# Performance work log

Measured on AMD Instinct MI355X. Metric: run time of the kernel, lower is better.

## Reference

```python
import jax, jax.numpy as jnp
import numpy as np

PATCH = 3  # patch_size=3, stride=1
B, C, H, W = 8, 256, 64, 64


def _extract_patches(x):
    # x: (c, h, w) -> (c*PATCH*PATCH, N) with N = (h-2)*(w-2), valid 3x3 patches
    c, h, w = x.shape
    hh, ww = h - PATCH + 1, w - PATCH + 1
    pats = jnp.stack([x[:, i:i + hh, j:j + ww]
                      for i in range(PATCH) for j in range(PATCH)], axis=0)  # (9, c, hh, ww)
    return pats.reshape(PATCH * PATCH * c, hh * ww)


def _index_to_flow(max_idx):
    # max_idx: (hh, ww) int -> flow (h, w, 2) padded by 2 at bottom/right
    hh, ww = max_idx.shape
    flow_w = (max_idx % ww).astype(jnp.float32)
    flow_h = (max_idx // ww).astype(jnp.float32)
    gy, gx = jnp.meshgrid(jnp.arange(hh, dtype=jnp.float32),
                          jnp.arange(ww, dtype=jnp.float32), indexing='ij')
    flow = jnp.stack((flow_w - gx, flow_h - gy), axis=2)  # (hh, ww, 2)
    return jnp.pad(flow, ((0, 2), (0, 2), (0, 0)))


def _per_image(feat_in, feat_ref):
    c, h, w = feat_in.shape
    hh, ww = h - PATCH + 1, w - PATCH + 1
    # channel-wise L2 normalize each spatial position (F.normalize dim=0, eps=1e-12)
    feat_in = feat_in / jnp.maximum(jnp.linalg.norm(feat_in, axis=0, keepdims=True), 1e-12)
    feat_ref = feat_ref / jnp.maximum(jnp.linalg.norm(feat_ref, axis=0, keepdims=True), 1e-12)
    Pi = _extract_patches(feat_in)    # (k, N)
    Pr = _extract_patches(feat_ref)   # (k, N)
    # is_norm=True: normalize ref patches (norm + 1e-5, per BasicSR feature_match_index)
    Pr = Pr / (jnp.linalg.norm(Pr, axis=0, keepdims=True) + 1e-5)
    corr = Pi.T @ Pr                  # (N, N) exhaustive patch correlation
    max_val = corr.max(axis=1)
    max_idx = jnp.argmax(corr, axis=1)
    # norm_input=True: divide by input patch norms
    max_val = max_val / jnp.linalg.norm(Pi, axis=0)
    max_val = max_val.reshape(hh, ww)
    max_idx = max_idx.reshape(hh, ww)
    sim = jnp.pad(max_val, ((1, 1), (1, 1)))[None]  # (1, h, w)
    flow = _index_to_flow(max_idx)                   # (h, w, 2)
    # nine down-right shifts (fill 0 at top-left), tensor_shift semantics
    shifted = jnp.stack([jnp.pad(flow[:h - i, :w - j], ((i, 0), (j, 0), (0, 0)))
                         for i in range(3) for j in range(3)], axis=0)  # (9, h, w, 2)
    return flow, shifted, sim


def setup_inputs() -> dict:
    key = jax.random.key(0)
    k1, k2 = jax.random.split(key)
    features1 = jax.random.normal(k1, (B, C, H, W), dtype=jnp.float32)
    features2 = jax.random.normal(k2, (B, C, H, W), dtype=jnp.float32)
    return {"features1": features1, "features2": features2}


def reference(features1, features2):
    pre_flow, pre_offset, pre_similarity = jax.vmap(_per_image)(features1, features2)
    # pre_flow: (b,h,w,2); pre_offset: (b,9,h,w,2); pre_similarity: (b,1,h,w)
    return pre_flow, pre_offset, pre_similarity
```

## Files before the change

kernel.cpp:

```cpp
#include <hip/hip_runtime.h>

typedef unsigned short u16;
typedef unsigned char u8;
typedef unsigned int u32;
typedef __bf16 bf16x8 __attribute__((ext_vector_type(8)));
typedef float f32x4 __attribute__((ext_vector_type(4)));

constexpr int BATCH = 8;
constexpr int C = 256;
constexpr int H = 64;
constexpr int W = 64;
constexpr int HW = H * W;
constexpr int HH = 62, WW = 62;
constexpr int NQ = HH * WW;
constexpr int SEG = 8;
constexpr int NBLK_RED = 536;

constexpr size_t OFF_RNORM = 0;
constexpr size_t OFF_RESV = 262144;
constexpr size_t OFF_RESI = 385280;
constexpr size_t OFF_SLOT0 = 508416;
constexpr size_t SP_H1 = 0;
constexpr size_t SP_L1 = 2097152;
constexpr size_t SP_H2 = 4194304;
constexpr size_t SP_L2 = 6291456;
constexpr size_t SP_P = 8388608;
constexpr size_t SP_PIDX8 = 75497472;
constexpr size_t SLOT_BYTES = 77594624;

typedef const __attribute__((address_space(1))) unsigned int* gas_ptr;
typedef __attribute__((address_space(3))) unsigned int* las_ptr;
__device__ __forceinline__ void gl16(const void* g, void* l) {
  __builtin_amdgcn_global_load_lds((gas_ptr)g, (las_ptr)l, 16, 0, 0);
}

__device__ __forceinline__ int pre_of(int ki) {
  if (ki <= 62) return ki * (ki + 1) / 2;
  int r = 123 - ki;
  return 1953 + 1891 - r * (r + 1) / 2;
}

__global__ __launch_bounds__(256) void norm_kernel(const float* __restrict__ f1,
                                                   const float* __restrict__ f2,
                                                   float* __restrict__ rnorm) {
  int by = blockIdx.x;
  int tensor = blockIdx.y;
  const float* f = tensor ? f2 : f1;
  int b = by >> 6, y = by & 63;
  int x = threadIdx.x & 63;
  int cq = threadIdx.x >> 6;
  const float* base = f + ((size_t)b * C) * HW + y * W + x;
  float s = 0.f;
  for (int c = cq; c < C; c += 4) {
    float v = base[(size_t)c * HW];
    s = fmaf(v, v, s);
  }
  __shared__ float sm[4][64];
  sm[cq][x] = s;
  __syncthreads();
  if (threadIdx.x < 64) {
    float t = sm[0][x] + sm[1][x] + sm[2][x] + sm[3][x];
    float nrm = fmaxf(sqrtf(t), 1e-12f);
    rnorm[((size_t)tensor * BATCH + b) * HW + y * W + x] = 1.0f / nrm;
  }
}

__global__ __launch_bounds__(256) void convert_kernel(const float* __restrict__ f1,
                                                      const float* __restrict__ f2,
                                                      const float* __restrict__ rnorm,
                                                      int b0, char* __restrict__ slot0) {
  int chunk = blockIdx.x;
  int tensor = blockIdx.y;
  int sloti = blockIdx.z;
  int bi = b0 + sloti;
  char* slot = slot0 + (size_t)sloti * SLOT_BYTES;
  int pos0 = chunk * 32;
  const float* f = (tensor ? f2 : f1) + (size_t)bi * C * HW;
  const float* rn = rnorm + ((size_t)tensor * BATCH + bi) * HW + pos0;
  u16* dh = (u16*)(slot + (tensor ? SP_H2 : SP_H1)) + (size_t)pos0 * C;
  u16* dl = (u16*)(slot + (tensor ? SP_L2 : SP_L1)) + (size_t)pos0 * C;

  __shared__ u32 sm[32][257];
  int t = threadIdx.x;
  int px = t & 31, cg = t >> 5;
  float r = rn[px];
  for (int kk = 0; kk < 32; ++kk) {
    int c = (cg << 5) + kk;
    float v = f[(size_t)c * HW + pos0 + px] * r;
    __bf16 h = (__bf16)v;
    float hf = (float)h;
    __bf16 lo = (__bf16)(v - hf);
    sm[px][c] = ((u32)__builtin_bit_cast(u16, h) << 16) | (u32)__builtin_bit_cast(u16, lo);
  }
  __syncthreads();
  int px2 = t >> 3, seg = t & 7;
  int c0 = seg * 32;
  for (int g8 = 0; g8 < 4; ++g8) {
    u32 hw0, hw1, hw2, hw3, lw0, lw1, lw2, lw3;
    u32 a, b2;
    a = sm[px2][c0 + g8 * 8 + 0]; b2 = sm[px2][c0 + g8 * 8 + 1];
    hw0 = (a >> 16) | (b2 & 0xFFFF0000u); lw0 = (a & 0xFFFFu) | (b2 << 16);
    a = sm[px2][c0 + g8 * 8 + 2]; b2 = sm[px2][c0 + g8 * 8 + 3];
    hw1 = (a >> 16) | (b2 & 0xFFFF0000u); lw1 = (a & 0xFFFFu) | (b2 << 16);
    a = sm[px2][c0 + g8 * 8 + 4]; b2 = sm[px2][c0 + g8 * 8 + 5];
    hw2 = (a >> 16) | (b2 & 0xFFFF0000u); lw2 = (a & 0xFFFFu) | (b2 << 16);
    a = sm[px2][c0 + g8 * 8 + 6]; b2 = sm[px2][c0 + g8 * 8 + 7];
    hw3 = (a >> 16) | (b2 & 0xFFFF0000u); lw3 = (a & 0xFFFFu) | (b2 << 16);
    size_t off = (size_t)px2 * C + c0 + g8 * 8;
    uint4 hv; hv.x = hw0; hv.y = hw1; hv.z = hw2; hv.w = hw3;
    uint4 lv; lv.x = lw0; lv.y = lw1; lv.z = lw2; lv.w = lw3;
    *(uint4*)(dh + off) = hv;
    *(uint4*)(dl + off) = lv;
  }
}

__global__ __launch_bounds__(256, 2) void pgemm_kernel(char* __restrict__ slot0) {
  char* slot = slot0 + (size_t)blockIdx.y * SLOT_BYTES;
  const u16* hi1 = (const u16*)(slot + SP_H1);
  const u16* lo1 = (const u16*)(slot + SP_L1);
  const u16* hi2 = (const u16*)(slot + SP_H2);
  const u16* lo2 = (const u16*)(slot + SP_L2);
  float* P = (float*)(slot + SP_P);

  int bid = blockIdx.x;
  int swz = (bid & 7) * 128 + (bid >> 3);
  int p0 = (swz >> 5) << 7, q0 = (swz & 31) << 7;

  __shared__ __align__(16) char smem[65536];
  char* sAh = smem;
  char* sAl = smem + 16384;
  char* sBh = smem + 32768;
  char* sBl = smem + 49152;

  int t = threadIdx.x;
  int l = t & 63, w = t >> 6, wm = w >> 1, wn = w & 1;
  int lr = l & 15, lh = l >> 4;
  int wv = w;

  const u16* src0 = hi1 + (size_t)p0 * 256;
  const u16* src1 = lo1 + (size_t)p0 * 256;
  const u16* src2 = hi2 + (size_t)q0 * 256;
  const u16* src3 = lo2 + (size_t)q0 * 256;

  f32x4 acc[4][4];
#pragma unroll
  for (int mf = 0; mf < 4; ++mf)
#pragma unroll
    for (int nf = 0; nf < 4; ++nf)
      acc[mf][nf] = (f32x4){0.f, 0.f, 0.f, 0.f};

  for (int kt = 0; kt < 4; ++kt) {
    if (kt) __syncthreads();
#pragma unroll
    for (int qq = 0; qq < 4; ++qq) {
      int q = wv * 4 + qq;
      int row = q * 8 + (l >> 3);
      int cc = l & 7;
      size_t goff = (size_t)row * 256 + kt * 64 + ((cc ^ (row & 7)) << 3);
      gl16(src0 + goff, sAh + q * 1024);
      gl16(src1 + goff, sAl + q * 1024);
      gl16(src2 + goff, sBh + q * 1024);
      gl16(src3 + goff, sBl + q * 1024);
    }
    __syncthreads();
#pragma unroll
    for (int ks = 0; ks < 2; ++ks) {
      bf16x8 ah[4], al[4];
#pragma unroll
      for (int mf = 0; mf < 4; ++mf) {
        int row = wm * 64 + mf * 16 + lr;
        int off = row * 128 + ((((ks * 4 + lh) << 4)) ^ ((row & 7) << 4));
        ah[mf] = *(const bf16x8*)(sAh + off);
        al[mf] = *(const bf16x8*)(sAl + off);
      }
#pragma unroll
      for (int nf = 0; nf < 4; ++nf) {
        int row = wn * 64 + nf * 16 + lr;
        int off = row * 128 + ((((ks * 4 + lh) << 4)) ^ ((row & 7) << 4));
        bf16x8 bh = *(const bf16x8*)(sBh + off);
        bf16x8 bl = *(const bf16x8*)(sBl + off);
#pragma unroll
        for (int mf = 0; mf < 4; ++mf) {
          acc[mf][nf] = __builtin_amdgcn_mfma_f32_16x16x32_bf16(ah[mf], bh, acc[mf][nf], 0, 0, 0);
          acc[mf][nf] = __builtin_amdgcn_mfma_f32_16x16x32_bf16(al[mf], bh, acc[mf][nf], 0, 0, 0);
          acc[mf][nf] = __builtin_amdgcn_mfma_f32_16x16x32_bf16(ah[mf], bl, acc[mf][nf], 0, 0, 0);
        }
      }
    }
  }

  __syncthreads();
  float* sq = (float*)smem;
#pragma unroll
  for (int pass = 0; pass < 2; ++pass) {
    if (pass) __syncthreads();
    if (wn == pass) {
      float* buf = sq + wm * 4352;
#pragma unroll
      for (int mf = 0; mf < 4; ++mf)
#pragma unroll
        for (int nf = 0; nf < 4; ++nf)
#pragma unroll
          for (int j = 0; j < 4; ++j)
            buf[(mf * 16 + lh * 4 + j) * 68 + nf * 16 + lr] = acc[mf][nf][j];
      *(f32x4*)(buf + l * 68 + 64) = (f32x4){0.f, 0.f, 0.f, 0.f};
    }
    __syncthreads();
    int tid2 = t & 127, sel = t >> 7;
    int ax = tid2 & 63, halfj = tid2 >> 6;
    const float* S = sq + sel * 4352;
    int rr1 = ax + 1 > 63 ? 63 : ax + 1;
    int rr2 = ax + 2 > 63 ? 63 : ax + 2;
    const float* S0 = S + ax * 68;
    const float* S1 = S + rr1 * 68;
    const float* S2 = S + rr2 * 68;
    int planeIdx = (((p0 >> 6) + sel) << 6) + (q0 >> 6) + pass;
    float* Qg = P + (((size_t)planeIdx) << 12) + ax * 8;
#pragma unroll
    for (int gi = 0; gi < 4; ++gi) {
      int g = halfj * 4 + gi;
      int c0 = g * 8;
      float r0[12], r1a[12], r2a[12];
#pragma unroll
      for (int u = 0; u < 3; ++u) {
        *(f32x4*)(r0 + u * 4) = *(const f32x4*)(S0 + c0 + u * 4);
        *(f32x4*)(r1a + u * 4) = *(const f32x4*)(S1 + c0 + u * 4);
        *(f32x4*)(r2a + u * 4) = *(const f32x4*)(S2 + c0 + u * 4);
      }
      f32x4 qv0, qv1;
#pragma unroll
      for (int e = 0; e < 4; ++e) qv0[e] = r0[e] + r1a[e + 1] + r2a[e + 2];
#pragma unroll
      for (int e = 0; e < 4; ++e) qv1[e] = r0[e + 4] + r1a[e + 5] + r2a[e + 6];
      *(f32x4*)(Qg + (size_t)g * 512) = qv0;
      *(f32x4*)(Qg + (size_t)g * 512 + 4) = qv1;
    }
  }
}

__global__ __launch_bounds__(512) void reduce_kernel(char* __restrict__ slot0,
                                                     size_t slotBytes) {
  int slot = blockIdx.y;
  char* sb = slot0 + (size_t)slot * slotBytes;
  const float* QT = (const float*)(sb + SP_P);
  float* pval8 = (float*)sb;
  u8* pidx8 = (u8*)(sb + SP_PIDX8);

  int bid = blockIdx.x;
  int ki = 0;
  for (ki = 0; ki < 123; ++ki) {
    int d = ki - 61; if (d < 0) d = -d;
    int ns = (62 - d + SEG - 1) / SEG;
    if (bid < ns) break;
    bid -= ns;
  }
  int k = ki - 61;
  int ystart = k < 0 ? -k : 0;
  int yend = k > 0 ? 61 - k : 61;
  int y0 = ystart + bid * SEG;
  int y1 = y0 + SEG; if (y1 > yend + 1) y1 = yend + 1;
  int sid0 = pre_of(ki) + (y0 - ystart);
  int pmax = yend + 2;

  int t = threadIdx.x;
  int w = t >> 6, l = t & 63;

  float A[8], B[8], P0[8], P1[8], P2[8];

  auto ld = [&](int p, float* D) {
    const float* gp = QT + (((size_t)((p << 6) + (p + k))) << 12) + (w << 9) + (l << 3);
    *(f32x4*)(D) = *(const f32x4*)(gp);
    *(f32x4*)(D + 4) = *(const f32x4*)(gp + 4);
  };

  auto candstep = [&](int y, const float* D0, const float* D1, const float* D2) {
    float best = __uint_as_float(0xFF800000u);
    int bbb = 0;
#pragma unroll
    for (int s = 0; s < 8; ++s) {
      float c = D0[s] + D1[s] + D2[s];
      bool valid = (w * 8 + s) <= 61;
      if (valid && c > best) { best = c; bbb = s; }
    }
    size_t o = (size_t)(sid0 + (y - y0)) * 512 + (w << 6) + l;
    pval8[o] = best;
    pidx8[o] = (u8)bbb;
  };

  ld(y0, A);
  ld(y0 + 1, B);
  ld(y0 + 2, P0);
  ld(y0 + 3 > pmax ? pmax : y0 + 3, P1);
  ld(y0 + 4 > pmax ? pmax : y0 + 4, P2);

  int y = y0;
  while (true) {
    candstep(y, A, B, P0);
#pragma unroll
    for (int s = 0; s < 8; ++s) { A[s] = B[s]; B[s] = P0[s]; }
    if (++y >= y1) break;
    ld(y + 4 > pmax ? pmax : y + 4, P0);
    candstep(y, A, B, P1);
#pragma unroll
    for (int s = 0; s < 8; ++s) { A[s] = B[s]; B[s] = P1[s]; }
    if (++y >= y1) break;
    ld(y + 4 > pmax ? pmax : y + 4, P1);
    candstep(y, A, B, P2);
#pragma unroll
    for (int s = 0; s < 8; ++s) { A[s] = B[s]; B[s] = P2[s]; }
    if (++y >= y1) break;
    ld(y + 4 > pmax ? pmax : y + 4, P2);
  }
}

__global__ __launch_bounds__(256) void combine_kernel(const char* __restrict__ slot0,
                                                      size_t slotBytes, int b0,
                                                      float* __restrict__ resv,
                                                      int* __restrict__ residx) {
  int q = blockIdx.x * 256 + threadIdx.x;
  if (q >= NQ) return;
  int slot = blockIdx.y;
  int b = b0 + slot;
  const char* sb = slot0 + (size_t)slot * slotBytes;
  const float* pval8 = (const float*)sb;
  const u8* pidx8 = (const u8*)(sb + SP_PIDX8);
  int y = q / 62, ax = q - y * 62;
  float best = __uint_as_float(0xFF800000u);
  int bjy = 0, bw = 0;
  for (int jy = 0; jy < 62; ++jy) {
    int ki = 61 + jy - y;
    int sid = pre_of(ki) + (y < jy ? y : jy);
    const float* p = pval8 + (size_t)sid * 512 + ax;
#pragma unroll
    for (int ww = 0; ww < 8; ++ww) {
      float v = p[ww << 6];
      if (v > best) { best = v; bjy = jy; bw = ww; }
    }
  }
  int kib = 61 + bjy - y;
  int sidb = pre_of(kib) + (y < bjy ? y : bjy);
  int bb = pidx8[(size_t)sidb * 512 + (bw << 6) + ax];
  resv[(size_t)b * NQ + q] = best;
  residx[(size_t)b * NQ + q] = bjy * 62 + bw * 8 + bb;
}

__global__ __launch_bounds__(256) void assemble_kernel(const float* __restrict__ res_val,
                                                       const int* __restrict__ res_idx,
                                                       float* __restrict__ out) {
  int gid = blockIdx.x * 256 + threadIdx.x;
  if (gid >= BATCH * HW) return;
  int b = gid >> 12;
  int y = (gid >> 6) & 63;
  int x = gid & 63;

  float* out_flow = out;
  float* out_off = out + (size_t)BATCH * HW * 2;
  float* out_sim = out + (size_t)BATCH * HW * 2 + (size_t)BATCH * 9 * HW * 2;

  auto flow_at = [&](int yy, int xx, float* fx, float* fy) {
    if (yy >= 0 && yy < HH && xx >= 0 && xx < WW) {
      int idx = res_idx[(size_t)b * NQ + yy * WW + xx];
      *fx = (float)(idx % WW - xx);
      *fy = (float)(idx / WW - yy);
    } else {
      *fx = 0.f;
      *fy = 0.f;
    }
  };

  float fx, fy;
  flow_at(y, x, &fx, &fy);
  size_t fo = ((size_t)b * HW + y * W + x) * 2;
  out_flow[fo + 0] = fx;
  out_flow[fo + 1] = fy;

#pragma unroll
  for (int sft = 0; sft < 9; ++sft) {
    int i = sft / 3, j = sft % 3;
    float ox, oy;
    flow_at(y - i, x - j, &ox, &oy);
    size_t o = (((size_t)b * 9 + sft) * HW + y * W + x) * 2;
    out_off[o + 0] = ox;
    out_off[o + 1] = oy;
  }

  float sim = 0.f;
  if (y >= 1 && y <= HH && x >= 1 && x <= WW) {
    float mv = res_val[(size_t)b * NQ + (y - 1) * WW + (x - 1)];
    sim = mv * (1.0f / ((3.0f + 1e-5f) * 3.0f));
  }
  out_sim[(size_t)b * HW + y * W + x] = sim;
}

extern "C" void kernel_launch(void* const* d_in, const int* in_sizes, int n_in,
                              void* d_out, int out_size, void* d_ws, size_t ws_size,
                              hipStream_t stream) {
  const float* f1 = (const float*)d_in[0];
  const float* f2 = (const float*)d_in[1];
  float* out = (float*)d_out;
  char* ws = (char*)d_ws;

  float* rnorm = (float*)(ws + OFF_RNORM);
  float* resv = (float*)(ws + OFF_RESV);
  int* residx = (int*)(ws + OFF_RESI);
  char* slot0 = ws + OFF_SLOT0;

  int nslots = 1;
  if (ws_size > OFF_SLOT0 + SLOT_BYTES) {
    size_t n = (ws_size - OFF_SLOT0) / SLOT_BYTES;
    nslots = n >= 8 ? 8 : (int)n;
    if (nslots < 1) nslots = 1;
  }

  norm_kernel<<<dim3(BATCH * H, 2), 256, 0, stream>>>(f1, f2, rnorm);

  for (int b0 = 0; b0 < BATCH; b0 += nslots) {
    int g = BATCH - b0 < nslots ? BATCH - b0 : nslots;
    convert_kernel<<<dim3(128, 2, g), 256, 0, stream>>>(f1, f2, rnorm, b0, slot0);
    pgemm_kernel<<<dim3(1024, g), 256, 0, stream>>>(slot0);
    reduce_kernel<<<dim3(NBLK_RED, g), 512, 0, stream>>>(slot0, SLOT_BYTES);
    combine_kernel<<<dim3(16, g), 256, 0, stream>>>(slot0, SLOT_BYTES, b0,
                                                    resv, residx);
  }

  int total = BATCH * HW;
  assemble_kernel<<<(total + 255) / 256, 256, 0, stream>>>(resv, residx, out);
}
```

Before: 551.2 us.

## Double-buffer GEMM K tiles in LDS and coalesce partial-sum plane stores

The GEMM main loop now uses two LDS buffers with a K-tile of 32, so the global-to-LDS load of the next tile is issued before the MFMAs on the current tile. This is meant to hide load latency behind compute, at the cost of twice as many K iterations and barriers. The layout of the partial-sum planes also changes: the two float4 halves are split 256 floats apart instead of being adjacent. Consecutive lanes therefore write and read contiguous 16-byte chunks, which should coalesce better in both the epilogue and the reduce kernel.

```diff
diff --git a/kernel.cpp b/kernel.cpp
--- a/kernel.cpp
+++ b/kernel.cpp
@@ -127,20 +127,13 @@
   int p0 = (swz >> 5) << 7, q0 = (swz & 31) << 7;
 
   __shared__ __align__(16) char smem[65536];
-  char* sAh = smem;
-  char* sAl = smem + 16384;
-  char* sBh = smem + 32768;
-  char* sBl = smem + 49152;
 
   int t = threadIdx.x;
   int l = t & 63, w = t >> 6, wm = w >> 1, wn = w & 1;
   int lr = l & 15, lh = l >> 4;
-  int wv = w;
-
-  const u16* src0 = hi1 + (size_t)p0 * 256;
-  const u16* src1 = lo1 + (size_t)p0 * 256;
-  const u16* src2 = hi2 + (size_t)q0 * 256;
-  const u16* src3 = lo2 + (size_t)q0 * 256;
+
+  const u16* srcs[4] = {hi1 + (size_t)p0 * 256, lo1 + (size_t)p0 * 256,
+                        hi2 + (size_t)q0 * 256, lo2 + (size_t)q0 * 256};
 
   f32x4 acc[4][4];
 #pragma unroll
@@ -149,47 +142,55 @@
     for (int nf = 0; nf < 4; ++nf)
       acc[mf][nf] = (f32x4){0.f, 0.f, 0.f, 0.f};
 
-  for (int kt = 0; kt < 4; ++kt) {
-    if (kt) __syncthreads();
-#pragma unroll
-    for (int qq = 0; qq < 4; ++qq) {
-      int q = wv * 4 + qq;
-      int row = q * 8 + (l >> 3);
-      int cc = l & 7;
-      size_t goff = (size_t)row * 256 + kt * 64 + ((cc ^ (row & 7)) << 3);
-      gl16(src0 + goff, sAh + q * 1024);
-      gl16(src1 + goff, sAl + q * 1024);
-      gl16(src2 + goff, sBh + q * 1024);
-      gl16(src3 + goff, sBl + q * 1024);
+  auto stage = [&](int b, int kt) {
+    char* base = smem + b * 32768;
+#pragma unroll
+    for (int pl = 0; pl < 4; ++pl) {
+      const u16* s = srcs[pl];
+#pragma unroll
+      for (int wq = 0; wq < 2; ++wq) {
+        int ci = (w * 2 + wq) * 64 + l;
+        int row = ci >> 2, cc = ci & 3;
+        size_t goff = (size_t)row * 256 + kt * 32 + ((cc ^ (row & 3)) << 3);
+        gl16(s + goff, base + pl * 8192 + (w * 2 + wq) * 1024 + l * 16);
+      }
+    }
+  };
+
+  stage(0, 0);
+  __syncthreads();
+
+  for (int kt = 0; kt < 8; ++kt) {
+    int b = kt & 1;
+    if (kt < 7) stage(b ^ 1, kt + 1);
+    char* sAh = smem + b * 32768;
+    char* sAl = sAh + 8192;
+    char* sBh = sAh + 16384;
+    char* sBl = sAh + 24576;
+    bf16x8 ah[4], al[4];
+#pragma unroll
+    for (int mf = 0; mf < 4; ++mf) {
+      int row = wm * 64 + mf * 16 + lr;
+      int off = row * 64 + (((lh) ^ (row & 3)) << 4);
+      ah[mf] = *(const bf16x8*)(sAh + off);
+      al[mf] = *(const bf16x8*)(sAl + off);
+    }
+#pragma unroll
+    for (int nf = 0; nf < 4; ++nf) {
+      int row = wn * 64 + nf * 16 + lr;
+      int off = row * 64 + (((lh) ^ (row & 3)) << 4);
+      bf16x8 bh = *(const bf16x8*)(sBh + off);
+      bf16x8 bl = *(const bf16x8*)(sBl + off);
+#pragma unroll
+      for (int mf = 0; mf < 4; ++mf) {
+        acc[mf][nf] = __builtin_amdgcn_mfma_f32_16x16x32_bf16(ah[mf], bh, acc[mf][nf], 0, 0, 0);
+        acc[mf][nf] = __builtin_amdgcn_mfma_f32_16x16x32_bf16(al[mf], bh, acc[mf][nf], 0, 0, 0);
+        acc[mf][nf] = __builtin_amdgcn_mfma_f32_16x16x32_bf16(ah[mf], bl, acc[mf][nf], 0, 0, 0);
+      }
     }
     __syncthreads();
-#pragma unroll
-    for (int ks = 0; ks < 2; ++ks) {
-      bf16x8 ah[4], al[4];
-#pragma unroll
-      for (int mf = 0; mf < 4; ++mf) {
-        int row = wm * 64 + mf * 16 + lr;
-        int off = row * 128 + ((((ks * 4 + lh) << 4)) ^ ((row & 7) << 4));
-        ah[mf] = *(const bf16x8*)(sAh + off);
-        al[mf] = *(const bf16x8*)(sAl + off);
-      }
-#pragma unroll
-      for (int nf = 0; nf < 4; ++nf) {
-        int row = wn * 64 + nf * 16 + lr;
-        int off = row * 128 + ((((ks * 4 + lh) << 4)) ^ ((row & 7) << 4));
-        bf16x8 bh = *(const bf16x8*)(sBh + off);
-        bf16x8 bl = *(const bf16x8*)(sBl + off);
-#pragma unroll
-        for (int mf = 0; mf < 4; ++mf) {
-          acc[mf][nf] = __builtin_amdgcn_mfma_f32_16x16x32_bf16(ah[mf], bh, acc[mf][nf], 0, 0, 0);
-          acc[mf][nf] = __builtin_amdgcn_mfma_f32_16x16x32_bf16(al[mf], bh, acc[mf][nf], 0, 0, 0);
-          acc[mf][nf] = __builtin_amdgcn_mfma_f32_16x16x32_bf16(ah[mf], bl, acc[mf][nf], 0, 0, 0);
-        }
-      }
-    }
-  }
-
-  __syncthreads();
+  }
+
   float* sq = (float*)smem;
 #pragma unroll
   for (int pass = 0; pass < 2; ++pass) {
@@ -215,7 +216,7 @@
     const float* S1 = S + rr1 * 68;
     const float* S2 = S + rr2 * 68;
     int planeIdx = (((p0 >> 6) + sel) << 6) + (q0 >> 6) + pass;
-    float* Qg = P + (((size_t)planeIdx) << 12) + ax * 8;
+    float* Qp = P + (((size_t)planeIdx) << 12);
 #pragma unroll
     for (int gi = 0; gi < 4; ++gi) {
       int g = halfj * 4 + gi;
@@ -232,8 +233,9 @@
       for (int e = 0; e < 4; ++e) qv0[e] = r0[e] + r1a[e + 1] + r2a[e + 2];
 #pragma unroll
       for (int e = 0; e < 4; ++e) qv1[e] = r0[e + 4] + r1a[e + 5] + r2a[e + 6];
-      *(f32x4*)(Qg + (size_t)g * 512) = qv0;
-      *(f32x4*)(Qg + (size_t)g * 512 + 4) = qv1;
+      float* Qg = Qp + g * 512 + (ax << 2);
+      *(f32x4*)(Qg) = qv0;
+      *(f32x4*)(Qg + 256) = qv1;
     }
   }
 }
@@ -268,9 +270,9 @@
   float A[8], B[8], P0[8], P1[8], P2[8];
 
   auto ld = [&](int p, float* D) {
-    const float* gp = QT + (((size_t)((p << 6) + (p + k))) << 12) + (w << 9) + (l << 3);
+    const float* gp = QT + (((size_t)((p << 6) + (p + k))) << 12) + (w << 9) + (l << 2);
     *(f32x4*)(D) = *(const f32x4*)(gp);
-    *(f32x4*)(D + 4) = *(const f32x4*)(gp + 4);
+    *(f32x4*)(D + 4) = *(const f32x4*)(gp + 256);
   };
 
   auto candstep = [&](int y, const float* D0, const float* D1, const float* D2) {
```

After: 540.7 us. No clear change (-1.9%).
